# Optimization experiments

Hardware: AMD Instinct MI355X
Metric: run time of the kernel (lower is better)

The kernel has to match this reference:

```python
import jax, jax.numpy as jnp
import numpy as np

DIM = 768
HEADS = 12
DIM_HEAD = 64
ROPE_BASE = 8192.0
LN_EPS = 1e-5


def setup_inputs() -> dict:
    key = jax.random.key(0)
    k1, k2, k3, k4 = jax.random.split(key, 4)
    B, N = 4, 2048
    x = jax.random.normal(k1, (B, N, DIM), dtype=jnp.float32)
    # 2D (time, pitch) coordinates in [0, 64)
    coords = jax.random.uniform(k2, (B, N, 2), dtype=jnp.float32) * 64.0
    ln_gamma = jnp.ones((DIM,), dtype=jnp.float32)
    ln_beta = jnp.zeros((DIM,), dtype=jnp.float32)
    w_qkv = jax.random.normal(k3, (3 * HEADS * DIM_HEAD, DIM), dtype=jnp.float32) * (DIM ** -0.5)
    w_out = jax.random.normal(k4, (DIM, HEADS * DIM_HEAD), dtype=jnp.float32) * ((HEADS * DIM_HEAD) ** -0.5)
    return {"x": x, "coords": coords, "ln_gamma": ln_gamma, "ln_beta": ln_beta,
            "w_qkv": w_qkv, "w_out": w_out}


def _rotate(t, cos, sin):
    # t: [B,H,N,ad]; cos/sin: [B,1,N,ad//2]
    t1 = t[..., 0::2]
    t2 = t[..., 1::2]
    return jnp.concatenate([t1 * cos - t2 * sin, t1 * sin + t2 * cos], axis=-1)


def _axis_cos_sin(coord, axis_dim):
    # coord: [B,N] -> cos/sin: [B,1,N,axis_dim//2]
    half = axis_dim // 2
    exp = jnp.arange(half, dtype=jnp.float32) / half
    inv_freq = jnp.exp(-exp * jnp.log(jnp.float32(ROPE_BASE)))  # [half]
    freqs = coord[:, :, None] * inv_freq[None, None, :]  # [B,N,half]
    return jnp.cos(freqs)[:, None], jnp.sin(freqs)[:, None]


def reference(x, coords, ln_gamma, ln_beta, w_qkv, w_out):
    B, N, D = x.shape
    scale = DIM_HEAD ** -0.5

    # LayerNorm
    mu = jnp.mean(x, axis=-1, keepdims=True)
    var = jnp.mean((x - mu) ** 2, axis=-1, keepdims=True)
    xn = (x - mu) * jax.lax.rsqrt(var + LN_EPS) * ln_gamma + ln_beta

    # QKV projection: [B,N,3*H*dh]
    qkv = jnp.einsum('bnd,ed->bne', xn, w_qkv)
    q, k, v = jnp.split(qkv, 3, axis=-1)

    def to_heads(t):
        return t.reshape(B, N, HEADS, DIM_HEAD).transpose(0, 2, 1, 3)  # b h n d
    q, k, v = to_heads(q), to_heads(k), to_heads(v)

    # 2D axial RoPE: x-axis on dims [0:dh//2), y-axis on dims [dh//2:dh)
    half = DIM_HEAD // 2
    slices = [(0, (0, half)), (1, (half, DIM_HEAD))]
    for axis_idx, (lo, hi) in slices:
        cos, sin = _axis_cos_sin(coords[..., axis_idx], hi - lo)
        q = jnp.concatenate([q[..., :lo], _rotate(q[..., lo:hi], cos, sin), q[..., hi:]], axis=-1)
        k = jnp.concatenate([k[..., :lo], _rotate(k[..., lo:hi], cos, sin), k[..., hi:]], axis=-1)

    # Attention
    dots = jnp.einsum('bhnd,bhmd->bhnm', q, k) * scale
    attn = jax.nn.softmax(dots, axis=-1)
    out = jnp.einsum('bhnm,bhmd->bhnd', attn, v)
    out = out.transpose(0, 2, 1, 3).reshape(B, N, HEADS * DIM_HEAD)
    return jnp.einsum('bne,de->bnd', out, w_out)
```

## Files before the change

### kernel.cpp

```cpp
#include <hip/hip_runtime.h>

#define B_ 4
#define N_ 2048
#define D_ 768
#define H_ 12
#define DH_ 64
#define ROWS_ (B_*N_)
#define E3_ (3*D_)

typedef _Float16 f16;
typedef __attribute__((ext_vector_type(8))) _Float16 half8;
typedef __attribute__((ext_vector_type(4))) _Float16 half4;
typedef __attribute__((ext_vector_type(2))) _Float16 half2;
typedef __attribute__((ext_vector_type(4))) float floatx4;

__device__ __forceinline__ void gload_lds16(const void* g, void* lds){
  __builtin_amdgcn_global_load_lds(
      (const __attribute__((address_space(1))) unsigned int*)g,
      (__attribute__((address_space(3))) unsigned int*)lds, 16, 0, 0);
}

__global__ __launch_bounds__(256) void cvt_kernel(const float* __restrict__ srcA,
    f16* __restrict__ dstA, int n8a, const float* __restrict__ srcB,
    f16* __restrict__ dstB, int n8b){
  int i = blockIdx.x*256 + threadIdx.x;
  const float* src; f16* dst; int j;
  if (i < n8a){ src = srcA; dst = dstA; j = i; }
  else { j = i - n8a; if (j >= n8b) return; src = srcB; dst = dstB; }
  float4 a = ((const float4*)src)[2*j];
  float4 b = ((const float4*)src)[2*j+1];
  half8 h;
  h[0]=(f16)a.x; h[1]=(f16)a.y; h[2]=(f16)a.z; h[3]=(f16)a.w;
  h[4]=(f16)b.x; h[5]=(f16)b.y; h[6]=(f16)b.z; h[7]=(f16)b.w;
  *(half8*)(dst + (size_t)j*8) = h;
}

__global__ __launch_bounds__(256) void ln_kernel(const float* __restrict__ x,
    const float* __restrict__ g, const float* __restrict__ be, f16* __restrict__ xn){
  int w = threadIdx.x >> 6, lane = threadIdx.x & 63;
  int row = blockIdx.x*4 + w;
  const float* xr = x + (size_t)row * D_;
  int c = lane*4;
  float4 f0 = *(const float4*)(xr + c);
  float4 f1 = *(const float4*)(xr + c + 256);
  float4 f2 = *(const float4*)(xr + c + 512);
  float s  = (f0.x+f0.y+f0.z+f0.w) + (f1.x+f1.y+f1.z+f1.w) + (f2.x+f2.y+f2.z+f2.w);
  float ss = (f0.x*f0.x+f0.y*f0.y+f0.z*f0.z+f0.w*f0.w)
           + (f1.x*f1.x+f1.y*f1.y+f1.z*f1.z+f1.w*f1.w)
           + (f2.x*f2.x+f2.y*f2.y+f2.z*f2.z+f2.w*f2.w);
  #pragma unroll
  for(int off=1; off<64; off<<=1){
    s  += __shfl_xor(s,  off, 64);
    ss += __shfl_xor(ss, off, 64);
  }
  float mean = s * (1.0f/D_);
  float var  = ss * (1.0f/D_) - mean*mean;
  float rstd = rsqrtf(var + 1e-5f);
  f16* xo = xn + (size_t)row * D_;
  #pragma unroll
  for(int part=0; part<3; ++part){
    float4 v = part==0 ? f0 : (part==1 ? f1 : f2);
    float4 gg = *(const float4*)(g  + c + part*256);
    float4 bb = *(const float4*)(be + c + part*256);
    half4 o;
    o[0] = (f16)((v.x-mean)*rstd*gg.x + bb.x);
    o[1] = (f16)((v.y-mean)*rstd*gg.y + bb.y);
    o[2] = (f16)((v.z-mean)*rstd*gg.z + bb.z);
    o[3] = (f16)((v.w-mean)*rstd*gg.w + bb.w);
    *(half4*)(xo + c + part*256) = o;
  }
}

__global__ __launch_bounds__(256) void rope_tab_kernel(const float* __restrict__ coords,
    float* __restrict__ T){
  int i = blockIdx.x*256 + threadIdx.x;
  int token = i >> 5, ax = (i >> 4) & 1, m = i & 15;
  float coord = coords[(size_t)token*2 + ax];
  float fr = exp2f((float)m * (-13.0f/16.0f));
  float sn, cs;
  sincosf(coord * fr, &sn, &cs);
  T[(size_t)token*64 + ax*32 + m]      = cs;
  T[(size_t)token*64 + ax*32 + 16 + m] = sn;
}

__global__ __launch_bounds__(256) void qkv_gemm(const f16* __restrict__ A,
    const f16* __restrict__ W, const float* __restrict__ T,
    f16* __restrict__ Q, f16* __restrict__ Kt, f16* __restrict__ VT){
  __shared__ __align__(16) char smem[128*136*2];
  f16* sA = (f16*)smem;
  f16* sB = (f16*)(smem + 16384);
  f16* sT = (f16*)smem;
  int tid = threadIdx.x;
  int w = tid >> 6, lane = tid & 63, quad = lane >> 4, l15 = lane & 15;
  int row0 = blockIdx.y * 128;
  int e0   = blockIdx.x * 128;
  int wr = (w >> 1) * 64, wc = (w & 1) * 64;
  int r8 = lane >> 3;
  int sc16 = ((lane & 7) ^ r8) * 8;
  int sw = l15 & 7;
  floatx4 acc[4][4];
  #pragma unroll
  for(int i=0;i<4;++i)
    #pragma unroll
    for(int j=0;j<4;++j) acc[i][j] = (floatx4){0.f,0.f,0.f,0.f};

  for(int k0=0; k0<D_; k0+=64){
    __syncthreads();
    #pragma unroll
    for(int j=0;j<4;++j){
      int rr = j*32 + w*8 + r8;
      gload_lds16(A + (size_t)(row0+rr)*D_ + k0 + sc16, sA + (j*32 + w*8)*64);
      gload_lds16(W + (size_t)(e0 +rr)*D_ + k0 + sc16, sB + (j*32 + w*8)*64);
    }
    __syncthreads();
    #pragma unroll
    for(int kk=0;kk<2;++kk){
      half8 af[4], bf[4];
      #pragma unroll
      for(int mi=0;mi<4;++mi)
        af[mi] = *(const half8*)&sA[(wr + mi*16 + l15)*64 + (((kk*4 + quad) ^ sw) << 3)];
      #pragma unroll
      for(int ni=0;ni<4;++ni)
        bf[ni] = *(const half8*)&sB[(wc + ni*16 + l15)*64 + (((kk*4 + quad) ^ sw) << 3)];
      #pragma unroll
      for(int mi=0;mi<4;++mi)
        #pragma unroll
        for(int ni=0;ni<4;++ni)
          acc[mi][ni] = __builtin_amdgcn_mfma_f32_16x16x32_f16(af[mi], bf[ni], acc[mi][ni], 0, 0, 0);
    }
  }
  int part = e0 / D_;
  int erel = e0 % D_;
  if (part == 2){
    #pragma unroll
    for(int ni=0;ni<4;++ni){
      int col = erel + wc + ni*16 + l15;
      int h = col >> 6, d = col & 63;
      #pragma unroll
      for(int mi=0;mi<4;++mi){
        int rbase = row0 + wr + mi*16 + quad*4;
        int b = rbase >> 11, n = rbase & 2047;
        half4 h4;
        #pragma unroll
        for(int reg=0;reg<4;++reg) h4[reg] = (f16)acc[mi][ni][reg];
        *(half4*)&VT[(((size_t)b*H_ + h)*DH_ + d)*N_ + n] = h4;
      }
    }
    return;
  }
  __syncthreads();
  #pragma unroll
  for(int mi=0;mi<4;++mi){
    int r = wr + mi*16 + quad*4;
    #pragma unroll
    for(int ni=0;ni<4;++ni){
      int c = wc + ni*16 + l15;
      #pragma unroll
      for(int reg=0;reg<4;++reg)
        sT[(size_t)(r+reg)*136 + c] = (f16)acc[mi][ni][reg];
    }
  }
  __syncthreads();
  int r  = tid >> 1;
  int hh = tid & 1;
  int n_global = row0 + r;
  const float* tt = T + (size_t)n_global*64;
  float tv[64];
  #pragma unroll
  for(int j=0;j<16;++j) *(float4*)&tv[j*4] = *(const float4*)(tt + j*4);
  f16 v[64];
  #pragma unroll
  for(int j=0;j<8;++j) *(half8*)&v[j*8] = *(const half8*)&sT[(size_t)r*136 + hh*64 + j*8];
  f16 o[64];
  #pragma unroll
  for(int ax=0; ax<2; ++ax){
    #pragma unroll
    for(int m=0;m<16;++m){
      float cs = tv[ax*32 + m];
      float sn = tv[ax*32 + 16 + m];
      float t1 = (float)v[ax*32 + 2*m];
      float t2 = (float)v[ax*32 + 2*m + 1];
      o[ax*32 + m]      = (f16)(t1*cs - t2*sn);
      o[ax*32 + 16 + m] = (f16)(t1*sn + t2*cs);
    }
  }
  int h = erel/64 + hh;
  int b = n_global >> 11, n = n_global & 2047;
  f16* dst = (part==0) ? Q : Kt;
  f16* op = dst + (((size_t)b*H_ + h)*N_ + n)*DH_;
  #pragma unroll
  for(int j=0;j<8;++j) *(half8*)(op + j*8) = *(half8*)&o[j*8];
}

__global__ __launch_bounds__(256, 3) void attn_kernel(const f16* __restrict__ Q,
    const f16* __restrict__ K, const f16* __restrict__ VT, f16* __restrict__ AO){
  __shared__ f16 sK[2][64*64];
  __shared__ f16 sV[2][64*64];
  __shared__ f16 sP[4][2][16*64];
  int bh = blockIdx.y;
  int q0 = blockIdx.x * 128;
  int tid = threadIdx.x;
  int w = tid >> 6, lane = tid & 63, quad = lane >> 4, l15 = lane & 15;
  const f16* Qb = Q  + (size_t)bh*N_*DH_;
  const f16* Ks = K  + (size_t)bh*N_*DH_;
  const f16* Vb = VT + (size_t)bh*DH_*N_;

  int r8 = lane >> 3;
  int swsrc = ((lane & 7) ^ r8) * 8;
  const f16* kst0 = Ks + (size_t)(w*16 +     r8)*DH_ + swsrc;
  const f16* kst1 = Ks + (size_t)(w*16 + 8 + r8)*DH_ + swsrc;
  const f16* vst0 = Vb + (size_t)(w*16 +     r8)*N_  + swsrc;
  const f16* vst1 = Vb + (size_t)(w*16 + 8 + r8)*N_  + swsrc;

  half8 qf0[2], qf1[2];
  #pragma unroll
  for(int s2=0;s2<2;++s2){
    const f16* qrow = Qb + (size_t)(q0 + 32*w + 16*s2 + l15)*DH_ + quad*8;
    qf0[s2] = *(const half8*)(qrow);
    qf1[s2] = *(const half8*)(qrow + 32);
    half8 cs8;
    #pragma unroll
    for(int j=0;j<8;++j) cs8[j] = (f16)0.18033688f;
    qf0[s2] = qf0[s2] * cs8;
    qf1[s2] = qf1[s2] * cs8;
  }

  gload_lds16(kst0, &sK[0][(w*16    )*64]);
  gload_lds16(kst1, &sK[0][(w*16 + 8)*64]);
  gload_lds16(vst0, &sV[0][(w*16    )*64]);
  gload_lds16(vst1, &sV[0][(w*16 + 8)*64]);
  kst0 += 64*DH_; kst1 += 64*DH_; vst0 += 64; vst1 += 64;

  float l_run[2] = {0.0f, 0.0f};
  floatx4 acc[2][4];
  #pragma unroll
  for(int s2=0;s2<2;++s2)
    #pragma unroll
    for(int dt=0;dt<4;++dt) acc[s2][dt] = (floatx4){0.f,0.f,0.f,0.f};
  __syncthreads();

  int sw = l15 & 7;
  f16* Prow[2] = { &sP[w][0][l15*64], &sP[w][1][l15*64] };

  const floatx4 SINIT = (floatx4){-8.f,-8.f,-8.f,-8.f};

#define ATTN_BODY(CUR, NXT) { \
    gload_lds16(kst0, &sK[NXT][(w*16    )*64]); \
    gload_lds16(kst1, &sK[NXT][(w*16 + 8)*64]); \
    gload_lds16(vst0, &sV[NXT][(w*16    )*64]); \
    gload_lds16(vst1, &sV[NXT][(w*16 + 8)*64]); \
    kst0 += 64*DH_; kst1 += 64*DH_; vst0 += 64; vst1 += 64; \
    const f16* sk = &sK[CUR][0]; \
    half8 kf0[4], kf1[4]; \
    _Pragma("unroll") \
    for(int nt=0;nt<4;++nt){ \
      int rr = 16*nt + l15; \
      kf0[nt] = *(const half8*)&sk[rr*64 + ((quad       ^ sw) << 3)]; \
      kf1[nt] = *(const half8*)&sk[rr*64 + (((quad + 4) ^ sw) << 3)]; \
    } \
    floatx4 s_[2][4]; \
    _Pragma("unroll") \
    for(int s2=0;s2<2;++s2) \
      _Pragma("unroll") \
      for(int nt=0; nt<4; ++nt){ \
        floatx4 z = SINIT; \
        z = __builtin_amdgcn_mfma_f32_16x16x32_f16(kf0[nt], qf0[s2], z, 0, 0, 0); \
        z = __builtin_amdgcn_mfma_f32_16x16x32_f16(kf1[nt], qf1[s2], z, 0, 0, 0); \
        s_[s2][nt] = z; \
      } \
    _Pragma("unroll") \
    for(int s2=0;s2<2;++s2){ \
      f16* Pb = Prow[s2]; \
      float r4[4]; \
      _Pragma("unroll") \
      for(int nt=0;nt<4;++nt){ \
        float p0 = __builtin_amdgcn_exp2f(s_[s2][nt][0]); \
        float p1 = __builtin_amdgcn_exp2f(s_[s2][nt][1]); \
        float p2 = __builtin_amdgcn_exp2f(s_[s2][nt][2]); \
        float p3 = __builtin_amdgcn_exp2f(s_[s2][nt][3]); \
        auto lo_ = __builtin_amdgcn_cvt_pkrtz(p0, p1); \
        auto hi_ = __builtin_amdgcn_cvt_pkrtz(p2, p3); \
        half2 lo, hi; \
        __builtin_memcpy(&lo, &lo_, 4);  __builtin_memcpy(&hi, &hi_, 4); \
        half4 h = __builtin_shufflevector(lo, hi, 0, 1, 2, 3); \
        *(half4*)&Pb[(((2*nt + (quad>>1)) ^ sw) << 3) + ((quad & 1) << 2)] = h; \
        r4[nt] = (p0+p1)+(p2+p3); \
      } \
      l_run[s2] += (r4[0]+r4[1])+(r4[2]+r4[3]); \
    } \
    { \
      const f16* sv = &sV[CUR][0]; \
      half8 pf0a = *(const half8*)&Prow[0][((quad       ^ sw) << 3)]; \
      half8 pf1a = *(const half8*)&Prow[0][(((4 + quad) ^ sw) << 3)]; \
      half8 pf0b = *(const half8*)&Prow[1][((quad       ^ sw) << 3)]; \
      half8 pf1b = *(const half8*)&Prow[1][(((4 + quad) ^ sw) << 3)]; \
      _Pragma("unroll") \
      for(int dt=0;dt<4;++dt){ \
        int rr = 16*dt + l15; \
        half8 v0 = *(const half8*)&sv[rr*64 + ((quad       ^ sw) << 3)]; \
        half8 v1 = *(const half8*)&sv[rr*64 + (((quad + 4) ^ sw) << 3)]; \
        acc[0][dt] = __builtin_amdgcn_mfma_f32_16x16x32_f16(v0, pf0a, acc[0][dt], 0, 0, 0); \
        acc[0][dt] = __builtin_amdgcn_mfma_f32_16x16x32_f16(v1, pf1a, acc[0][dt], 0, 0, 0); \
        acc[1][dt] = __builtin_amdgcn_mfma_f32_16x16x32_f16(v0, pf0b, acc[1][dt], 0, 0, 0); \
        acc[1][dt] = __builtin_amdgcn_mfma_f32_16x16x32_f16(v1, pf1b, acc[1][dt], 0, 0, 0); \
      } \
    } \
    __syncthreads(); \
  }

  #pragma unroll 1
  for(int t=0; t<N_/128; ++t){
    ATTN_BODY(0, 1);
    ATTN_BODY(1, 0);
  }
#undef ATTN_BODY

  int b = bh / H_, h = bh % H_;
  #pragma unroll
  for(int s2=0;s2<2;++s2){
    float l = l_run[s2];
    l += __shfl_xor(l, 16, 64);
    l += __shfl_xor(l, 32, 64);
    float inv = 1.0f / l;
    f16* Pb = Prow[s2];
    #pragma unroll
    for(int dt=0;dt<4;++dt){
      half4 h4;
      h4[0]=(f16)(acc[s2][dt][0]*inv); h4[1]=(f16)(acc[s2][dt][1]*inv);
      h4[2]=(f16)(acc[s2][dt][2]*inv); h4[3]=(f16)(acc[s2][dt][3]*inv);
      *(half4*)&Pb[(((2*dt + (quad>>1)) ^ sw) << 3) + ((quad & 1) << 2)] = h4;
    }
    half8 o0 = *(const half8*)&Pb[(((2*quad    ) ^ sw) << 3)];
    half8 o1 = *(const half8*)&Pb[(((2*quad + 1) ^ sw) << 3)];
    f16* op = AO + ((size_t)(b*N_ + q0 + 32*w + 16*s2 + l15))*D_ + h*DH_ + quad*16;
    *(half8*)(op)     = o0;
    *(half8*)(op + 8) = o1;
  }
}

__global__ __launch_bounds__(256) void out_gemm(const f16* __restrict__ A,
    const f16* __restrict__ W, float* __restrict__ C){
  __shared__ f16 sA[128*64];
  __shared__ f16 sB[128*64];
  int tid = threadIdx.x;
  int w = tid >> 6, lane = tid & 63, quad = lane >> 4, l15 = lane & 15;
  int row0 = blockIdx.y * 128;
  int e0   = blockIdx.x * 128;
  int wr = (w >> 1) * 64, wc = (w & 1) * 64;
  int r8 = lane >> 3;
  int sc16 = ((lane & 7) ^ r8) * 8;
  int sw = l15 & 7;
  floatx4 acc[4][4];
  #pragma unroll
  for(int i=0;i<4;++i)
    #pragma unroll
    for(int j=0;j<4;++j) acc[i][j] = (floatx4){0.f,0.f,0.f,0.f};

  for(int k0=0; k0<D_; k0+=64){
    __syncthreads();
    #pragma unroll
    for(int j=0;j<4;++j){
      int rr = j*32 + w*8 + r8;
      gload_lds16(A + (size_t)(row0+rr)*D_ + k0 + sc16, sA + (j*32 + w*8)*64);
      gload_lds16(W + (size_t)(e0 +rr)*D_ + k0 + sc16, sB + (j*32 + w*8)*64);
    }
    __syncthreads();
    #pragma unroll
    for(int kk=0;kk<2;++kk){
      half8 af[4], bf[4];
      #pragma unroll
      for(int mi=0;mi<4;++mi)
        af[mi] = *(const half8*)&sA[(wr + mi*16 + l15)*64 + (((kk*4 + quad) ^ sw) << 3)];
      #pragma unroll
      for(int ni=0;ni<4;++ni)
        bf[ni] = *(const half8*)&sB[(wc + ni*16 + l15)*64 + (((kk*4 + quad) ^ sw) << 3)];
      #pragma unroll
      for(int mi=0;mi<4;++mi)
        #pragma unroll
        for(int ni=0;ni<4;++ni)
          acc[mi][ni] = __builtin_amdgcn_mfma_f32_16x16x32_f16(af[mi], bf[ni], acc[mi][ni], 0, 0, 0);
    }
  }
  #pragma unroll
  for(int ni=0;ni<4;++ni){
    int col = e0 + wc + ni*16 + l15;
    #pragma unroll
    for(int mi=0;mi<4;++mi){
      int rbase = row0 + wr + mi*16 + quad*4;
      #pragma unroll
      for(int reg=0;reg<4;++reg)
        C[(size_t)(rbase+reg)*D_ + col] = acc[mi][ni][reg];
    }
  }
}

extern "C" void kernel_launch(void* const* d_in, const int* in_sizes, int n_in,
                              void* d_out, int out_size, void* d_ws, size_t ws_size,
                              hipStream_t stream) {
  (void)in_sizes; (void)n_in; (void)out_size; (void)ws_size;
  const float* x      = (const float*)d_in[0];
  const float* coords = (const float*)d_in[1];
  const float* g      = (const float*)d_in[2];
  const float* be     = (const float*)d_in[3];
  const float* wqkv   = (const float*)d_in[4];
  const float* wout   = (const float*)d_in[5];
  float* out = (float*)d_out;
  char* ws = (char*)d_ws;
  const size_t SEG = (size_t)ROWS_ * D_ * 2;
  f16* xn  = (f16*)(ws + 0*SEG);
  f16* Q   = (f16*)(ws + 1*SEG);
  f16* K   = (f16*)(ws + 2*SEG);
  f16* VT  = (f16*)(ws + 3*SEG);
  f16* AO  = (f16*)(ws + 4*SEG);
  f16* W16 = (f16*)(ws + 5*SEG);
  f16* Wo16= (f16*)(ws + 5*SEG + (size_t)E3_*D_*2);
  float* T = (float*)AO;

  const int n8a = E3_*D_/8, n8b = D_*D_/8;
  cvt_kernel <<<(n8a+n8b+255)/256, 256, 0, stream>>>(wqkv, W16, n8a, wout, Wo16, n8b);
  ln_kernel  <<<ROWS_/4, 256, 0, stream>>>(x, g, be, xn);
  rope_tab_kernel<<<(B_*N_*32)/256, 256, 0, stream>>>(coords, T);
  qkv_gemm   <<<dim3(E3_/128, ROWS_/128), 256, 0, stream>>>(xn, W16, T, Q, K, VT);
  attn_kernel<<<dim3(N_/128, B_*H_), 256, 0, stream>>>(Q, K, VT, AO);
  out_gemm   <<<dim3(D_/128, ROWS_/128), 256, 0, stream>>>(AO, Wo16, out);
}
```

Baseline: 275.8 us.

## Stage V transpose via LDS and switch attention K/V loads to register prefetch

The QKV GEMM epilogue for the V part now goes through shared memory, so each thread writes 64 contiguous n-values of VT with 16-byte stores instead of scattered 8-byte stores. The attention kernel drops global_load_lds direct-to-LDS copies. Instead it loads the next K/V tile into registers at the top of each iteration and writes it to the swizzled LDS buffer after the compute, before the barrier. This trades asynchronous LDS DMA for register-staged prefetch, which adds register pressure under a launch bound of 3 blocks per CU.

```diff
diff --git a/kernel.cpp b/kernel.cpp
--- a/kernel.cpp
+++ b/kernel.cpp
@@ -132,20 +132,31 @@
   int part = e0 / D_;
   int erel = e0 % D_;
   if (part == 2){
-    #pragma unroll
-    for(int ni=0;ni<4;++ni){
-      int col = erel + wc + ni*16 + l15;
-      int h = col >> 6, d = col & 63;
-      #pragma unroll
-      for(int mi=0;mi<4;++mi){
-        int rbase = row0 + wr + mi*16 + quad*4;
-        int b = rbase >> 11, n = rbase & 2047;
-        half4 h4;
+    __syncthreads();
+    #pragma unroll
+    for(int mi=0;mi<4;++mi){
+      int r = wr + mi*16 + quad*4;
+      #pragma unroll
+      for(int ni=0;ni<4;++ni){
+        int c = wc + ni*16 + l15;
         #pragma unroll
-        for(int reg=0;reg<4;++reg) h4[reg] = (f16)acc[mi][ni][reg];
-        *(half4*)&VT[(((size_t)b*H_ + h)*DH_ + d)*N_ + n] = h4;
+        for(int reg=0;reg<4;++reg)
+          sT[(size_t)(r+reg)*136 + c] = (f16)acc[mi][ni][reg];
       }
     }
+    __syncthreads();
+    int colT = tid >> 1;
+    int nh   = (tid & 1) * 64;
+    int h = erel/64 + (colT >> 6);
+    int d = colT & 63;
+    int rbase = row0 + nh;
+    int b = rbase >> 11, n = rbase & 2047;
+    f16 tmp[64];
+    #pragma unroll
+    for(int j=0;j<64;++j) tmp[j] = sT[(size_t)(nh + j)*136 + colT];
+    f16* op = VT + (((size_t)b*H_ + h)*DH_ + d)*N_ + n;
+    #pragma unroll
+    for(int j=0;j<8;++j) *(half8*)(op + j*8) = *(half8*)&tmp[j*8];
     return;
   }
   __syncthreads();
@@ -205,12 +216,11 @@
   const f16* Ks = K  + (size_t)bh*N_*DH_;
   const f16* Vb = VT + (size_t)bh*DH_*N_;
 
-  int r8 = lane >> 3;
-  int swsrc = ((lane & 7) ^ r8) * 8;
-  const f16* kst0 = Ks + (size_t)(w*16 +     r8)*DH_ + swsrc;
-  const f16* kst1 = Ks + (size_t)(w*16 + 8 + r8)*DH_ + swsrc;
-  const f16* vst0 = Vb + (size_t)(w*16 +     r8)*N_  + swsrc;
-  const f16* vst1 = Vb + (size_t)(w*16 + 8 + r8)*N_  + swsrc;
+  int sd = tid >> 2, sc = tid & 3;
+  const f16* vp = Vb + (size_t)sd*N_ + sc*16;
+  const f16* kp = Ks + (size_t)sd*DH_ + sc*16;
+  int sw0 = sd*64 + (((2*sc    ) ^ (sd & 7)) << 3);
+  int sw1 = sd*64 + (((2*sc + 1) ^ (sd & 7)) << 3);
 
   half8 qf0[2], qf1[2];
   #pragma unroll
@@ -225,11 +235,15 @@
     qf1[s2] = qf1[s2] * cs8;
   }
 
-  gload_lds16(kst0, &sK[0][(w*16    )*64]);
-  gload_lds16(kst1, &sK[0][(w*16 + 8)*64]);
-  gload_lds16(vst0, &sV[0][(w*16    )*64]);
-  gload_lds16(vst1, &sV[0][(w*16 + 8)*64]);
-  kst0 += 64*DH_; kst1 += 64*DH_; vst0 += 64; vst1 += 64;
+  {
+    half8 k0 = *(const half8*)(kp);
+    half8 k1 = *(const half8*)(kp + 8);
+    half8 g0 = *(const half8*)(vp);
+    half8 g1 = *(const half8*)(vp + 8);
+    *(half8*)&sK[0][sw0] = k0;  *(half8*)&sK[0][sw1] = k1;
+    *(half8*)&sV[0][sw0] = g0;  *(half8*)&sV[0][sw1] = g1;
+  }
+  kp += 64*DH_;  vp += 64;
 
   float l_run[2] = {0.0f, 0.0f};
   floatx4 acc[2][4];
@@ -245,11 +259,9 @@
   const floatx4 SINIT = (floatx4){-8.f,-8.f,-8.f,-8.f};
 
 #define ATTN_BODY(CUR, NXT) { \
-    gload_lds16(kst0, &sK[NXT][(w*16    )*64]); \
-    gload_lds16(kst1, &sK[NXT][(w*16 + 8)*64]); \
-    gload_lds16(vst0, &sV[NXT][(w*16    )*64]); \
-    gload_lds16(vst1, &sV[NXT][(w*16 + 8)*64]); \
-    kst0 += 64*DH_; kst1 += 64*DH_; vst0 += 64; vst1 += 64; \
+    half8 nk0 = *(const half8*)(kp);      half8 nk1 = *(const half8*)(kp + 8); \
+    half8 ng0 = *(const half8*)(vp);      half8 ng1 = *(const half8*)(vp + 8); \
+    kp += 64*DH_;  vp += 64; \
     const f16* sk = &sK[CUR][0]; \
     half8 kf0[4], kf1[4]; \
     _Pragma("unroll") \
@@ -305,6 +317,12 @@
         acc[1][dt] = __builtin_amdgcn_mfma_f32_16x16x32_f16(v1, pf1b, acc[1][dt], 0, 0, 0); \
       } \
     } \
+    { \
+      f16* dk = &sK[NXT][0]; \
+      f16* dv = &sV[NXT][0]; \
+      *(half8*)&dk[sw0] = nk0;  *(half8*)&dk[sw1] = nk1; \
+      *(half8*)&dv[sw0] = ng0;  *(half8*)&dv[sw1] = ng1; \
+    } \
     __syncthreads(); \
   }
 
```

After: 237.8 us. 13.8% less time.
